# Optimization experiments

Hardware: AMD Instinct MI355X
Metric: run time of the kernel (lower is better)

The kernel has to match this reference:

```python
import jax, jax.numpy as jnp
import numpy as np

IN_DIM = 512
POS_RFACTOR = 8
MAX_POS = 128
WP = MAX_POS // POS_RFACTOR  # pooled 1D width = 16


def _sin_table(max_len, d):
    # HANet-style sinusoidal table; row 0 is all zeros
    pos = np.arange(max_len)[:, None].astype(np.float64)
    j = np.arange(d)[None, :]
    angle = pos / np.power(10000.0, 2 * (j // 2) / d)
    enc = np.zeros((max_len, d), dtype=np.float32)
    enc[1:, 0::2] = np.sin(angle[1:, 0::2])
    enc[1:, 1::2] = np.cos(angle[1:, 1::2])
    return jnp.asarray(enc)


def setup_inputs() -> dict:
    key = jax.random.key(0)
    ks = jax.random.split(key, 6)
    B, C, H, W = 4, IN_DIM, 64, 64
    Ck = C // 2
    s = 1.0 / np.sqrt(C)
    return {
        "x": jax.random.normal(ks[0], (B, C, H, W), jnp.float32),
        "Wq": jax.random.normal(ks[1], (Ck, C), jnp.float32) * s,
        "bq": jnp.zeros((Ck,), jnp.float32),
        "Wk": jax.random.normal(ks[2], (Ck, C), jnp.float32) * s,
        "bk": jnp.zeros((Ck,), jnp.float32),
        "Wv": jax.random.normal(ks[3], (C, C), jnp.float32) * s,
        "bv": jnp.zeros((C,), jnp.float32),
        "gamma": jnp.ones((1,), jnp.float32),  # torch inits to 0; nonzero here so output/grads are non-trivial
        "pe_table": _sin_table(MAX_POS, C),
        "pos": jax.random.randint(ks[4], (B, H, W), 0, MAX_POS, dtype=jnp.int32),
    }


def reference(x, Wq, bq, Wk, bk, Wv, bv, gamma, pe_table, pos):
    B, C, H, W = x.shape
    # colpool: AdaptiveAvgPool2d((1, WP)) -> mean over H, block-mean over W (W % WP == 0)
    x1d = x.mean(axis=2).reshape(B, C, WP, W // WP).mean(axis=-1)  # B,C,WP
    # PosEncoding1D (eval mode, no noise): select first row, //rfactor, nearest-resize to WP, embed
    p = pos[:, 0, :] // POS_RFACTOR                 # B,W
    nidx = (jnp.arange(WP) * W) // WP               # nearest-neighbor indices
    pe = pe_table[p[:, nidx]]                       # B,WP,C
    x1d = x1d + jnp.transpose(pe, (0, 2, 1))        # B,C,WP
    # Upsample(x1d.unsqueeze(2), (H,W)): bilinear align_corners=True; height dim is 1 -> constant
    src = jnp.arange(W, dtype=jnp.float32) * (WP - 1) / (W - 1)
    i0 = jnp.floor(src).astype(jnp.int32)
    i1 = jnp.minimum(i0 + 1, WP - 1)
    t = (src - i0.astype(jnp.float32)).astype(x.dtype)
    row = x1d[:, :, i0] * (1.0 - t) + x1d[:, :, i1] * t  # B,C,W
    x2d = jnp.broadcast_to(row[:, :, None, :], (B, C, H, W))
    # 1x1 conv projections
    q = jnp.einsum('bchw,oc->bohw', x, Wq) + bq[None, :, None, None]
    k = jnp.einsum('bchw,oc->bohw', x2d, Wk) + bk[None, :, None, None]
    v = jnp.einsum('bchw,oc->bohw', x, Wv) + bv[None, :, None, None]
    N = H * W
    q = q.reshape(B, -1, N)   # B,Ck,N
    k = k.reshape(B, -1, N)   # B,Ck,N
    v = v.reshape(B, C, N)    # B,C,N
    energy = jnp.einsum('bcn,bcm->bnm', q, k)        # B,N,N (query n, key m), unscaled
    attn = jax.nn.softmax(energy, axis=-1)
    out = jnp.einsum('bcm,bnm->bcn', v, attn)        # B,C,N
    out = out.reshape(B, C, H, W)
    return gamma[0] * out + x
```

## Files before the change

### kernel.cpp

```cpp
#include <hip/hip_runtime.h>

#define CDIM 512
#define OKD  256
#define NDIM 4096

#define OFF_XMH 0
#define OFF_X1  131072
#define OFF_K1  163840
#define OFF_M1A 180224
#define OFF_CB1 196608
#define OFF_VMB 196672

typedef float f32x4  __attribute__((ext_vector_type(4)));
typedef short shortx4 __attribute__((ext_vector_type(4)));
typedef short shortx8 __attribute__((ext_vector_type(8)));

static __device__ __forceinline__ unsigned short f2bf(float f) {
  unsigned u = __float_as_uint(f);
  u = (u + 0x7FFFu + ((u >> 16) & 1u)) >> 16;
  return (unsigned short)u;
}
static __device__ __forceinline__ unsigned pk2(float lo, float hi) {
  return (unsigned)f2bf(lo) | ((unsigned)f2bf(hi) << 16);
}

__global__ __launch_bounds__(256) void k_reduce(const float* __restrict__ x,
                                                const float* __restrict__ pe,
                                                const int* __restrict__ pos,
                                                float* __restrict__ xmh,
                                                float* __restrict__ x1pe) {
  int t = threadIdx.x;
  int bc = blockIdx.x * 4 + (t >> 6);
  int w4 = t & 15;
  int hoff = (t >> 4) & 3;
  const float4* xp = (const float4*)(x) + (size_t)bc * (64 * 16);
  float4 acc = make_float4(0.f, 0.f, 0.f, 0.f);
#pragma unroll
  for (int k = 0; k < 16; ++k) {
    float4 v = xp[(hoff + 4 * k) * 16 + w4];
    acc.x += v.x; acc.y += v.y; acc.z += v.z; acc.w += v.w;
  }
  acc.x += __shfl_xor(acc.x, 16); acc.y += __shfl_xor(acc.y, 16);
  acc.z += __shfl_xor(acc.z, 16); acc.w += __shfl_xor(acc.w, 16);
  acc.x += __shfl_xor(acc.x, 32); acc.y += __shfl_xor(acc.y, 32);
  acc.z += __shfl_xor(acc.z, 32); acc.w += __shfl_xor(acc.w, 32);
  if (hoff == 0) {
    const float inv = 1.f / 64.f;
    float4 o = make_float4(acc.x * inv, acc.y * inv, acc.z * inv, acc.w * inv);
    ((float4*)xmh)[bc * 16 + w4] = o;
    int b = bc >> 9;
    int c = bc & 511;
    int ps = pos[b * 4096 + 4 * w4] >> 3;
    float x1 = (o.x + o.y + o.z + o.w) * 0.25f + pe[ps * CDIM + c];
    x1pe[bc * 16 + w4] = x1;
  }
}

__global__ __launch_bounds__(128) void k_vmk1(const float* __restrict__ Wv,
                                              const float* __restrict__ bv,
                                              const float* __restrict__ Wk,
                                              const float* __restrict__ bk,
                                              const float* __restrict__ xmh,
                                              const float* __restrict__ x1pe,
                                              unsigned short* __restrict__ vmb,
                                              float* __restrict__ K1) {
  int t = threadIdx.x;
  int blk = blockIdx.x;
  if (blk < 64) {
    int wid = blk * 2 + (t >> 6);
    int lane = t & 63, nrel = lane & 15, kg = lane >> 4;
    int b = wid >> 5, rem = wid & 31, cgrp = rem >> 2, wt = rem & 3;
    f32x4 acc[4] = {{0,0,0,0},{0,0,0,0},{0,0,0,0},{0,0,0,0}};
    for (int kt = 0; kt < 16; ++kt) {
      const float* xp = xmh + (size_t)(b * 512 + kt * 32 + kg * 4) * 64 + wt * 16 + nrel;
      float v0 = xp[0], v1 = xp[64], v2 = xp[128], v3 = xp[192];
      float v4 = xp[1024], v5 = xp[1088], v6 = xp[1152], v7 = xp[1216];
      shortx8 bf;
      unsigned* bu = (unsigned*)&bf;
      bu[0] = pk2(v0, v1); bu[1] = pk2(v2, v3);
      bu[2] = pk2(v4, v5); bu[3] = pk2(v6, v7);
#pragma unroll
      for (int m = 0; m < 4; ++m) {
        int c = (cgrp * 4 + m) * 16 + nrel;
        const float* wp = Wv + (size_t)c * 512 + kt * 32 + kg * 4;
        float4 a0 = *(const float4*)wp;
        float4 a1 = *(const float4*)(wp + 16);
        shortx8 af;
        unsigned* au = (unsigned*)&af;
        au[0] = pk2(a0.x, a0.y); au[1] = pk2(a0.z, a0.w);
        au[2] = pk2(a1.x, a1.y); au[3] = pk2(a1.z, a1.w);
        acc[m] = __builtin_amdgcn_mfma_f32_16x16x32_bf16(af, bf, acc[m], 0, 0, 0);
      }
    }
#pragma unroll
    for (int m = 0; m < 4; ++m)
#pragma unroll
      for (int r = 0; r < 4; ++r) {
        int c = (cgrp * 4 + m) * 16 + kg * 4 + r;
        vmb[(size_t)(b * 512 + c) * 64 + wt * 16 + nrel] = f2bf(acc[m][r] + bv[c]);
      }
  } else {
    int idx = blk - 64;
    int b = idx >> 5, og = idx & 31;
    int o = og * 8 + (t >> 4), i = t & 15;
    const float* Wr = Wk + (size_t)o * 512;
    const float* xb = x1pe + ((size_t)b * 512) * 16 + i;
    float a0 = 0.f, a1 = 0.f, a2 = 0.f, a3 = 0.f;
    for (int c = 0; c < 512; c += 4) {
      a0 += Wr[c]     * xb[c * 16];
      a1 += Wr[c + 1] * xb[(c + 1) * 16];
      a2 += Wr[c + 2] * xb[(c + 2) * 16];
      a3 += Wr[c + 3] * xb[(c + 3) * 16];
    }
    K1[((b << 8) + o) * 16 + i] = bk[o] + a0 + a1 + a2 + a3;
  }
}

__global__ __launch_bounds__(256) void k_m1(const float* __restrict__ Wq,
                                            const float* __restrict__ bq,
                                            const float* __restrict__ K1,
                                            unsigned short* __restrict__ m1A,
                                            float* __restrict__ cb1) {
  int t = threadIdx.x;
  int blk = blockIdx.x;
  if (blk < 128) {
    int b = blk >> 5;
    int c = (blk & 31) * 16 + (t >> 4);
    int i = t & 15;
    const float* Wc = Wq + c;
    const float* Kb = K1 + (b << 8) * 16 + i;
    float a0 = 0.f, a1 = 0.f, a2 = 0.f, a3 = 0.f;
    for (int o = 0; o < OKD; o += 4) {
      a0 += Wc[o * CDIM]       * Kb[o * 16];
      a1 += Wc[(o + 1) * CDIM] * Kb[(o + 1) * 16];
      a2 += Wc[(o + 2) * CDIM] * Kb[(o + 2) * 16];
      a3 += Wc[(o + 3) * CDIM] * Kb[(o + 3) * 16];
    }
    float acc = a0 + a1 + a2 + a3;
    int kt = c >> 5, kl = c & 31;
    int kg = (kl < 16) ? (kl >> 2) : ((kl - 16) >> 2);
    int j  = (kl & 3) + ((kl < 16) ? 0 : 4);
    m1A[(size_t)b * 8192 + ((kt * 16 + i) * 4 + kg) * 8 + j] = f2bf(acc);
  } else if (t < 64) {
    int b = t >> 4, i = t & 15;
    const float* Kb = K1 + (b << 8) * 16 + i;
    float acc = 0.f;
    for (int o = 0; o < OKD; ++o) acc += bq[o] * Kb[o * 16];
    cb1[b * 16 + i] = acc;
  }
}

__global__ __launch_bounds__(512, 4) void k_attn(const float* __restrict__ x,
                                                 const unsigned short* __restrict__ m1A,
                                                 const float* __restrict__ cb1,
                                                 const unsigned short* __restrict__ vmb,
                                                 const float* __restrict__ gamma,
                                                 float* __restrict__ out) {
  __shared__ float e1w[8][32][17];
  __shared__ __align__(16) char p_t[4096];

  const int t = threadIdx.x;
  const int lane = t & 63;
  const int wv = t >> 6;
  const int b  = blockIdx.x >> 7;
  const int n0 = (blockIdx.x & 127) * 32;
  const int nrel = lane & 15;
  const int kg = lane >> 4;

  {
    f32x4 pacc[2] = {{0,0,0,0},{0,0,0,0}};
#pragma unroll
    for (int ktw = 0; ktw < 2; ++ktw) {
      int ktg = wv * 2 + ktw;
      shortx8 af = *(const shortx8*)(m1A + (size_t)b * 8192 +
                                     ((size_t)((ktg * 16 + nrel) * 4 + kg)) * 8);
#pragma unroll
      for (int nt = 0; nt < 2; ++nt) {
        const float* xp = x + (size_t)(b * 512 + wv * 64 + ktw * 32 + kg * 4) * NDIM +
                          n0 + nt * 16 + nrel;
        float v0 = xp[0],          v1 = xp[NDIM],        v2 = xp[2 * NDIM],  v3 = xp[3 * NDIM];
        float v4 = xp[16 * NDIM],  v5 = xp[17 * NDIM],   v6 = xp[18 * NDIM], v7 = xp[19 * NDIM];
        shortx8 bf;
        unsigned* bu = (unsigned*)&bf;
        bu[0] = pk2(v0, v1); bu[1] = pk2(v2, v3);
        bu[2] = pk2(v4, v5); bu[3] = pk2(v6, v7);
        pacc[nt] = __builtin_amdgcn_mfma_f32_16x16x32_bf16(af, bf, pacc[nt], 0, 0, 0);
      }
    }
#pragma unroll
    for (int nt = 0; nt < 2; ++nt)
#pragma unroll
      for (int r = 0; r < 4; ++r)
        e1w[wv][nt * 16 + nrel][kg * 4 + r] = pacc[nt][r];
  }
  __syncthreads();

  {
    const int sn = t >> 4;
    const int si = t & 15;
    float ev = cb1[b * 16 + si];
#pragma unroll
    for (int g = 0; g < 8; ++g) ev += e1w[g][sn][si];
    float pv[4];
    float mx = -3.4e38f;
#pragma unroll
    for (int j = 0; j < 4; ++j) {
      int w = si * 4 + j;
      float srcf = (float)w * (15.0f / 63.0f);
      int i0 = (int)srcf;
      float tf = srcf - (float)i0;
      int i1 = i0 + 1; if (i1 > 15) i1 = 15;
      float v0 = __shfl(ev, (lane & 48) | i0);
      float v1 = __shfl(ev, (lane & 48) | i1);
      float vv = v0 * (1.0f - tf) + v1 * tf;
      pv[j] = vv;
      mx = fmaxf(mx, vv);
    }
    mx = fmaxf(mx, __shfl_xor(mx, 1));
    mx = fmaxf(mx, __shfl_xor(mx, 2));
    mx = fmaxf(mx, __shfl_xor(mx, 4));
    mx = fmaxf(mx, __shfl_xor(mx, 8));
    float s = 0.f;
#pragma unroll
    for (int j = 0; j < 4; ++j) { pv[j] = __expf(pv[j] - mx); s += pv[j]; }
    s += __shfl_xor(s, 1); s += __shfl_xor(s, 2);
    s += __shfl_xor(s, 4); s += __shfl_xor(s, 8);
    float inv = 1.0f / s;
    unsigned lo = pk2(pv[0] * inv, pv[1] * inv);
    unsigned hi = pk2(pv[2] * inv, pv[3] * inv);
    unsigned* dst = (unsigned*)(p_t + sn * 128 + ((si ^ (sn & 15)) << 3));
    dst[0] = lo; dst[1] = hi;
  }
  __syncthreads();

  {
    const float gm = gamma[0];
#pragma unroll
    for (int j = 0; j < 8; ++j) {
      const int idx = wv * 8 + j;
      const int ct = idx >> 1, nt = idx & 1;
      f32x4 dacc = {0.f, 0.f, 0.f, 0.f};
      const unsigned short* vrow =
          vmb + ((size_t)(b * CDIM + ct * 16 + nrel)) * 64 + kg * 4;
      const char* prow = p_t + (nt * 16 + nrel) * 128;
#pragma unroll
      for (int ks = 0; ks < 2; ++ks) {
        shortx4 a0 = *(const shortx4*)(vrow + ks * 32);
        shortx4 a1 = *(const shortx4*)(vrow + ks * 32 + 16);
        shortx8 av = __builtin_shufflevector(a0, a1, 0, 1, 2, 3, 4, 5, 6, 7);
        int G0 = (ks * 8 + kg) ^ nrel;
        int G1 = (ks * 8 + 4 + kg) ^ nrel;
        shortx4 b0 = *(const shortx4*)(prow + G0 * 8);
        shortx4 b1 = *(const shortx4*)(prow + G1 * 8);
        shortx8 bv2 = __builtin_shufflevector(b0, b1, 0, 1, 2, 3, 4, 5, 6, 7);
        dacc = __builtin_amdgcn_mfma_f32_16x16x32_bf16(av, bv2, dacc, 0, 0, 0);
      }
#pragma unroll
      for (int r = 0; r < 4; ++r) {
        int c_o = ct * 16 + kg * 4 + r;
        size_t base = (size_t)(b * CDIM + c_o) * NDIM + n0 + nt * 16 + nrel;
        out[base] = gm * dacc[r] + x[base];
      }
    }
  }
}

extern "C" void kernel_launch(void* const* d_in, const int* in_sizes, int n_in,
                              void* d_out, int out_size, void* d_ws, size_t ws_size,
                              hipStream_t stream) {
  const float* x     = (const float*)d_in[0];
  const float* Wq    = (const float*)d_in[1];
  const float* bq    = (const float*)d_in[2];
  const float* Wk    = (const float*)d_in[3];
  const float* bk    = (const float*)d_in[4];
  const float* Wv    = (const float*)d_in[5];
  const float* bv    = (const float*)d_in[6];
  const float* gamma = (const float*)d_in[7];
  const float* pe    = (const float*)d_in[8];
  const int*   pos   = (const int*)d_in[9];
  float* out = (float*)d_out;
  float* ws  = (float*)d_ws;

  float* xmh  = ws + OFF_XMH;
  float* x1pe = ws + OFF_X1;
  float* K1   = ws + OFF_K1;
  unsigned short* m1A = (unsigned short*)(ws + OFF_M1A);
  float* cb1  = ws + OFF_CB1;
  unsigned short* vmb = (unsigned short*)(ws + OFF_VMB);

  hipLaunchKernelGGL(k_reduce, dim3(512), dim3(256), 0, stream, x, pe, pos, xmh, x1pe);
  hipLaunchKernelGGL(k_vmk1, dim3(192), dim3(128), 0, stream, Wv, bv, Wk, bk, xmh, x1pe, vmb, K1);
  hipLaunchKernelGGL(k_m1, dim3(129), dim3(256), 0, stream, Wq, bq, K1, m1A, cb1);
  hipLaunchKernelGGL(k_attn, dim3(512), dim3(512), 0, stream, x, m1A, cb1, vmb, gamma, out);
}
```

Measured before the change: 138.0 us.

## Precompute Wq^T·Wk weight product to merge four launches into three

Reassociates the query-key chain by computing G = Wq^T Wk (plus bias cross terms) from the weights alone, in the same launch as the spatial reduction. The next kernel then forms m1A directly as G times the pooled positional features with MFMA, which removes one dependent kernel launch and the serial K1 then m1A chain. The cost is a 512x512 weight-product GEMM that is recomputed on every call, plus extra bf16 rounding of G.

```diff
diff --git a/kernel.cpp b/kernel.cpp
--- a/kernel.cpp
+++ b/kernel.cpp
@@ -6,10 +6,13 @@
 
 #define OFF_XMH 0
 #define OFF_X1  131072
-#define OFF_K1  163840
-#define OFF_M1A 180224
-#define OFF_CB1 196608
-#define OFF_VMB 196672
+#define OFF_GA  163840
+#define OFF_GK  294912
+#define OFF_GB  295424
+#define OFF_SBB 295936
+#define OFF_CB1 296000
+#define OFF_M1A 296064
+#define OFF_VMB 312448
 
 typedef float f32x4  __attribute__((ext_vector_type(4)));
 typedef short shortx4 __attribute__((ext_vector_type(4)));
@@ -24,51 +27,117 @@
   return (unsigned)f2bf(lo) | ((unsigned)f2bf(hi) << 16);
 }
 
-__global__ __launch_bounds__(256) void k_reduce(const float* __restrict__ x,
-                                                const float* __restrict__ pe,
-                                                const int* __restrict__ pos,
-                                                float* __restrict__ xmh,
-                                                float* __restrict__ x1pe) {
-  int t = threadIdx.x;
-  int bc = blockIdx.x * 4 + (t >> 6);
-  int w4 = t & 15;
-  int hoff = (t >> 4) & 3;
-  const float4* xp = (const float4*)(x) + (size_t)bc * (64 * 16);
-  float4 acc = make_float4(0.f, 0.f, 0.f, 0.f);
-#pragma unroll
-  for (int k = 0; k < 16; ++k) {
-    float4 v = xp[(hoff + 4 * k) * 16 + w4];
-    acc.x += v.x; acc.y += v.y; acc.z += v.z; acc.w += v.w;
-  }
-  acc.x += __shfl_xor(acc.x, 16); acc.y += __shfl_xor(acc.y, 16);
-  acc.z += __shfl_xor(acc.z, 16); acc.w += __shfl_xor(acc.w, 16);
-  acc.x += __shfl_xor(acc.x, 32); acc.y += __shfl_xor(acc.y, 32);
-  acc.z += __shfl_xor(acc.z, 32); acc.w += __shfl_xor(acc.w, 32);
-  if (hoff == 0) {
-    const float inv = 1.f / 64.f;
-    float4 o = make_float4(acc.x * inv, acc.y * inv, acc.z * inv, acc.w * inv);
-    ((float4*)xmh)[bc * 16 + w4] = o;
-    int b = bc >> 9;
-    int c = bc & 511;
-    int ps = pos[b * 4096 + 4 * w4] >> 3;
-    float x1 = (o.x + o.y + o.z + o.w) * 0.25f + pe[ps * CDIM + c];
-    x1pe[bc * 16 + w4] = x1;
-  }
-}
-
-__global__ __launch_bounds__(128) void k_vmk1(const float* __restrict__ Wv,
-                                              const float* __restrict__ bv,
-                                              const float* __restrict__ Wk,
-                                              const float* __restrict__ bk,
-                                              const float* __restrict__ xmh,
-                                              const float* __restrict__ x1pe,
-                                              unsigned short* __restrict__ vmb,
-                                              float* __restrict__ K1) {
+__global__ __launch_bounds__(256) void k_pre(const float* __restrict__ x,
+                                             const float* __restrict__ pe,
+                                             const int* __restrict__ pos,
+                                             const float* __restrict__ Wq,
+                                             const float* __restrict__ Wk,
+                                             const float* __restrict__ bq,
+                                             const float* __restrict__ bk,
+                                             float* __restrict__ xmh,
+                                             float* __restrict__ x1pe,
+                                             unsigned short* __restrict__ gA,
+                                             float* __restrict__ gk,
+                                             float* __restrict__ gb,
+                                             float* __restrict__ sbb) {
+  __shared__ float wq_s[64][33];
+  __shared__ float wk_s[64][33];
   int t = threadIdx.x;
   int blk = blockIdx.x;
-  if (blk < 64) {
-    int wid = blk * 2 + (t >> 6);
-    int lane = t & 63, nrel = lane & 15, kg = lane >> 4;
+  if (blk < 512) {
+    int bc = blk * 4 + (t >> 6);
+    int w4 = t & 15;
+    int hoff = (t >> 4) & 3;
+    const float4* xp = (const float4*)(x) + (size_t)bc * (64 * 16);
+    float4 acc = make_float4(0.f, 0.f, 0.f, 0.f);
+#pragma unroll
+    for (int k = 0; k < 16; ++k) {
+      float4 v = xp[(hoff + 4 * k) * 16 + w4];
+      acc.x += v.x; acc.y += v.y; acc.z += v.z; acc.w += v.w;
+    }
+    acc.x += __shfl_xor(acc.x, 16); acc.y += __shfl_xor(acc.y, 16);
+    acc.z += __shfl_xor(acc.z, 16); acc.w += __shfl_xor(acc.w, 16);
+    acc.x += __shfl_xor(acc.x, 32); acc.y += __shfl_xor(acc.y, 32);
+    acc.z += __shfl_xor(acc.z, 32); acc.w += __shfl_xor(acc.w, 32);
+    if (hoff == 0) {
+      const float inv = 1.f / 64.f;
+      float4 o = make_float4(acc.x * inv, acc.y * inv, acc.z * inv, acc.w * inv);
+      ((float4*)xmh)[bc * 16 + w4] = o;
+      int b = bc >> 9;
+      int c = bc & 511;
+      int ps = pos[b * 4096 + 4 * w4] >> 3;
+      float x1 = (o.x + o.y + o.z + o.w) * 0.25f + pe[ps * CDIM + c];
+      x1pe[bc * 16 + w4] = x1;
+    }
+  } else if (blk < 768) {
+    int gi = blk - 512;
+    int c0  = (gi >> 4) * 32;
+    int cp0 = (gi & 15) * 32;
+    int tcp = t & 31;
+    int tcr = t >> 5;
+    float acc0 = 0.f, acc1 = 0.f, acc2 = 0.f, acc3 = 0.f;
+    for (int o0 = 0; o0 < OKD; o0 += 64) {
+      __syncthreads();
+      {
+        int row = t >> 2, col = (t & 3) * 8;
+        *(float4*)&wq_s[row][col]     = *(const float4*)&Wq[(size_t)(o0 + row) * CDIM + c0 + col];
+        *(float4*)&wq_s[row][col + 4] = *(const float4*)&Wq[(size_t)(o0 + row) * CDIM + c0 + col + 4];
+        *(float4*)&wk_s[row][col]     = *(const float4*)&Wk[(size_t)(o0 + row) * CDIM + cp0 + col];
+        *(float4*)&wk_s[row][col + 4] = *(const float4*)&Wk[(size_t)(o0 + row) * CDIM + cp0 + col + 4];
+      }
+      __syncthreads();
+#pragma unroll 8
+      for (int o = 0; o < 64; ++o) {
+        float wkv = wk_s[o][tcp];
+        acc0 += wq_s[o][tcr]      * wkv;
+        acc1 += wq_s[o][tcr + 8]  * wkv;
+        acc2 += wq_s[o][tcr + 16] * wkv;
+        acc3 += wq_s[o][tcr + 24] * wkv;
+      }
+    }
+    int cp = cp0 + tcp;
+    int ktp = cp >> 5, klp = cp & 31;
+    int kgp = (klp < 16) ? (klp >> 2) : ((klp - 16) >> 2);
+    int jp  = (klp & 3) + ((klp < 16) ? 0 : 4);
+    float av[4] = {acc0, acc1, acc2, acc3};
+#pragma unroll
+    for (int r = 0; r < 4; ++r) {
+      int c = c0 + tcr + r * 8;
+      gA[((size_t)(c * 16 + ktp) * 4 + kgp) * 8 + jp] = f2bf(av[r]);
+    }
+  } else {
+    for (int cc = t; cc < CDIM; cc += 256) {
+      float a = 0.f, b2 = 0.f;
+      for (int o = 0; o < OKD; ++o) {
+        a  += Wq[(size_t)o * CDIM + cc] * bk[o];
+        b2 += bq[o] * Wk[(size_t)o * CDIM + cc];
+      }
+      gk[cc] = a; gb[cc] = b2;
+    }
+    if (t == 0) {
+      float s = 0.f;
+      for (int o = 0; o < OKD; ++o) s += bq[o] * bk[o];
+      sbb[0] = s;
+    }
+  }
+}
+
+__global__ __launch_bounds__(256) void k_mid(const float* __restrict__ Wv,
+                                             const float* __restrict__ bv,
+                                             const float* __restrict__ xmh,
+                                             const float* __restrict__ x1pe,
+                                             const unsigned short* __restrict__ gA,
+                                             const float* __restrict__ gk,
+                                             const float* __restrict__ gb,
+                                             const float* __restrict__ sbb,
+                                             unsigned short* __restrict__ vmb,
+                                             unsigned short* __restrict__ m1A,
+                                             float* __restrict__ cb1) {
+  int t = threadIdx.x;
+  int blk = blockIdx.x;
+  int lane = t & 63, nrel = lane & 15, kg = lane >> 4;
+  if (blk < 32) {
+    int wid = blk * 4 + (t >> 6);
     int b = wid >> 5, rem = wid & 31, cgrp = rem >> 2, wt = rem & 3;
     f32x4 acc[4] = {{0,0,0,0},{0,0,0,0},{0,0,0,0},{0,0,0,0}};
     for (int kt = 0; kt < 16; ++kt) {
@@ -99,54 +168,45 @@
         int c = (cgrp * 4 + m) * 16 + kg * 4 + r;
         vmb[(size_t)(b * 512 + c) * 64 + wt * 16 + nrel] = f2bf(acc[m][r] + bv[c]);
       }
+  } else if (blk < 48) {
+    int idx = blk - 32;
+    int b = idx >> 2;
+    int wv = t >> 6;
+    int ct0 = (idx & 3) * 8 + wv * 2;
+#pragma unroll
+    for (int cti = 0; cti < 2; ++cti) {
+      int ct = ct0 + cti;
+      f32x4 acc = {0.f, 0.f, 0.f, 0.f};
+      for (int kt = 0; kt < 16; ++kt) {
+        shortx8 af = *(const shortx8*)(gA +
+            ((size_t)((ct * 16 + nrel) * 16 + kt) * 4 + kg) * 8);
+        const float* xp = x1pe + (size_t)(b * 512 + kt * 32 + kg * 4) * 16 + nrel;
+        float v0 = xp[0],   v1 = xp[16],  v2 = xp[32],  v3 = xp[48];
+        float v4 = xp[256], v5 = xp[272], v6 = xp[288], v7 = xp[304];
+        shortx8 bf;
+        unsigned* bu = (unsigned*)&bf;
+        bu[0] = pk2(v0, v1); bu[1] = pk2(v2, v3);
+        bu[2] = pk2(v4, v5); bu[3] = pk2(v6, v7);
+        acc = __builtin_amdgcn_mfma_f32_16x16x32_bf16(af, bf, acc, 0, 0, 0);
+      }
+#pragma unroll
+      for (int r = 0; r < 4; ++r) {
+        int c = ct * 16 + kg * 4 + r;
+        float val = acc[r] + gk[c];
+        int ktm = c >> 5, klm = c & 31;
+        int kgm = (klm < 16) ? (klm >> 2) : ((klm - 16) >> 2);
+        int jm = (klm & 3) + ((klm < 16) ? 0 : 4);
+        m1A[(size_t)b * 8192 + ((size_t)(ktm * 16 + nrel) * 4 + kgm) * 8 + jm] = f2bf(val);
+      }
+    }
   } else {
-    int idx = blk - 64;
-    int b = idx >> 5, og = idx & 31;
-    int o = og * 8 + (t >> 4), i = t & 15;
-    const float* Wr = Wk + (size_t)o * 512;
-    const float* xb = x1pe + ((size_t)b * 512) * 16 + i;
-    float a0 = 0.f, a1 = 0.f, a2 = 0.f, a3 = 0.f;
-    for (int c = 0; c < 512; c += 4) {
-      a0 += Wr[c]     * xb[c * 16];
-      a1 += Wr[c + 1] * xb[(c + 1) * 16];
-      a2 += Wr[c + 2] * xb[(c + 2) * 16];
-      a3 += Wr[c + 3] * xb[(c + 3) * 16];
-    }
-    K1[((b << 8) + o) * 16 + i] = bk[o] + a0 + a1 + a2 + a3;
-  }
-}
-
-__global__ __launch_bounds__(256) void k_m1(const float* __restrict__ Wq,
-                                            const float* __restrict__ bq,
-                                            const float* __restrict__ K1,
-                                            unsigned short* __restrict__ m1A,
-                                            float* __restrict__ cb1) {
-  int t = threadIdx.x;
-  int blk = blockIdx.x;
-  if (blk < 128) {
-    int b = blk >> 5;
-    int c = (blk & 31) * 16 + (t >> 4);
-    int i = t & 15;
-    const float* Wc = Wq + c;
-    const float* Kb = K1 + (b << 8) * 16 + i;
-    float a0 = 0.f, a1 = 0.f, a2 = 0.f, a3 = 0.f;
-    for (int o = 0; o < OKD; o += 4) {
-      a0 += Wc[o * CDIM]       * Kb[o * 16];
-      a1 += Wc[(o + 1) * CDIM] * Kb[(o + 1) * 16];
-      a2 += Wc[(o + 2) * CDIM] * Kb[(o + 2) * 16];
-      a3 += Wc[(o + 3) * CDIM] * Kb[(o + 3) * 16];
-    }
-    float acc = a0 + a1 + a2 + a3;
-    int kt = c >> 5, kl = c & 31;
-    int kg = (kl < 16) ? (kl >> 2) : ((kl - 16) >> 2);
-    int j  = (kl & 3) + ((kl < 16) ? 0 : 4);
-    m1A[(size_t)b * 8192 + ((kt * 16 + i) * 4 + kg) * 8 + j] = f2bf(acc);
-  } else if (t < 64) {
-    int b = t >> 4, i = t & 15;
-    const float* Kb = K1 + (b << 8) * 16 + i;
-    float acc = 0.f;
-    for (int o = 0; o < OKD; ++o) acc += bq[o] * Kb[o * 16];
-    cb1[b * 16 + i] = acc;
+    if (t < 64) {
+      int b = t >> 4, i = t & 15;
+      const float* xb = x1pe + ((size_t)b * 512) * 16 + i;
+      float a = sbb[0];
+      for (int c = 0; c < 512; ++c) a += gb[c] * xb[c * 16];
+      cb1[b * 16 + i] = a;
+    }
   }
 }
 
@@ -178,8 +238,8 @@
       for (int nt = 0; nt < 2; ++nt) {
         const float* xp = x + (size_t)(b * 512 + wv * 64 + ktw * 32 + kg * 4) * NDIM +
                           n0 + nt * 16 + nrel;
-        float v0 = xp[0],          v1 = xp[NDIM],        v2 = xp[2 * NDIM],  v3 = xp[3 * NDIM];
-        float v4 = xp[16 * NDIM],  v5 = xp[17 * NDIM],   v6 = xp[18 * NDIM], v7 = xp[19 * NDIM];
+        float v0 = xp[0],         v1 = xp[NDIM],       v2 = xp[2 * NDIM],  v3 = xp[3 * NDIM];
+        float v4 = xp[16 * NDIM], v5 = xp[17 * NDIM],  v6 = xp[18 * NDIM], v7 = xp[19 * NDIM];
         shortx8 bf;
         unsigned* bu = (unsigned*)&bf;
         bu[0] = pk2(v0, v1); bu[1] = pk2(v2, v3);
@@ -228,7 +288,7 @@
     float inv = 1.0f / s;
     unsigned lo = pk2(pv[0] * inv, pv[1] * inv);
     unsigned hi = pk2(pv[2] * inv, pv[3] * inv);
-    unsigned* dst = (unsigned*)(p_t + sn * 128 + ((si ^ (sn & 15)) << 3));
+    unsigned* dst = (unsigned*)(p_t + (t >> 4) * 128 + ((si ^ ((t >> 4) & 15)) << 3));
     dst[0] = lo; dst[1] = hi;
   }
   __syncthreads();
@@ -283,13 +343,18 @@
 
   float* xmh  = ws + OFF_XMH;
   float* x1pe = ws + OFF_X1;
-  float* K1   = ws + OFF_K1;
+  unsigned short* gA = (unsigned short*)(ws + OFF_GA);
+  float* gk   = ws + OFF_GK;
+  float* gb   = ws + OFF_GB;
+  float* sbb  = ws + OFF_SBB;
+  float* cb1  = ws + OFF_CB1;
   unsigned short* m1A = (unsigned short*)(ws + OFF_M1A);
-  float* cb1  = ws + OFF_CB1;
   unsigned short* vmb = (unsigned short*)(ws + OFF_VMB);
 
-  hipLaunchKernelGGL(k_reduce, dim3(512), dim3(256), 0, stream, x, pe, pos, xmh, x1pe);
-  hipLaunchKernelGGL(k_vmk1, dim3(192), dim3(128), 0, stream, Wv, bv, Wk, bk, xmh, x1pe, vmb, K1);
-  hipLaunchKernelGGL(k_m1, dim3(129), dim3(256), 0, stream, Wq, bq, K1, m1A, cb1);
-  hipLaunchKernelGGL(k_attn, dim3(512), dim3(512), 0, stream, x, m1A, cb1, vmb, gamma, out);
-}
+  hipLaunchKernelGGL(k_pre, dim3(769), dim3(256), 0, stream,
+                     x, pe, pos, Wq, Wk, bq, bk, xmh, x1pe, gA, gk, gb, sbb);
+  hipLaunchKernelGGL(k_mid, dim3(49), dim3(256), 0, stream,
+                     Wv, bv, xmh, x1pe, gA, gk, gb, sbb, vmb, m1A, cb1);
+  hipLaunchKernelGGL(k_attn, dim3(512), dim3(512), 0, stream,
+                     x, m1A, cb1, vmb, gamma, out);
+}
```

New measurement: 164.3 us. +19.0%, slower.
